# Optimization experiments

Measured on AMD Instinct MI355X. Metric: run time of the kernel, lower is better.

Reference implementation:

```python
import jax, jax.numpy as jnp
import numpy as np

MAX_LEN, BATCH, EMB = 512, 32, 41
HID, UNITS = 800, 20
BOND_LENS = jnp.array([1.329, 1.459, 1.525], jnp.float32)
BOND_ANGLES = jnp.array([2.034, 2.119, 1.937], jnp.float32)
INIT_ABC = jnp.array([[0.0, 0.0, 1.0], [0.0, 1.0, 0.0], [1.0, 0.0, 0.0]], jnp.float32)


def _lstm_dir(x, w_ih, w_hh, b, reverse):
    # x: [T, B, in]; returns hidden states [T, B, H]
    T, B, _ = x.shape
    H = w_hh.shape[1]
    xs = jnp.flip(x, 0) if reverse else x
    xw = jnp.einsum('tbi,gi->tbg', xs, w_ih) + b  # precompute input projection

    def step(carry, xt):
        h, c = carry
        gates = xt + h @ w_hh.T
        i, f, g, o = jnp.split(gates, 4, axis=-1)
        c = jax.nn.sigmoid(f) * c + jax.nn.sigmoid(i) * jnp.tanh(g)
        h = jax.nn.sigmoid(o) * jnp.tanh(c)
        return (h, c), h

    init = (jnp.zeros((B, H), x.dtype), jnp.zeros((B, H), x.dtype))
    _, hs = jax.lax.scan(step, init, xw)
    return jnp.flip(hs, 0) if reverse else hs


def _bilstm_layer(x, w_ih, w_hh, b):
    # w_ih: [2, 4H, in]; w_hh: [2, 4H, H]; b: [2, 4H]
    fwd = _lstm_dir(x, w_ih[0], w_hh[0], b[0], False)
    bwd = _lstm_dir(x, w_ih[1], w_hh[1], b[1], True)
    return jnp.concatenate([fwd, bwd], axis=-1)


def _geometric_unit(coords3, triplet):
    # coords3: [3, B, 3] last three atoms; triplet: [B, 3] torsion angles
    A, Bc, C = coords3[0], coords3[1], coords3[2]
    new = []
    for i in range(3):
        Tang, R, P = BOND_ANGLES[i], BOND_LENS[i], triplet[:, i]
        D2 = jnp.stack([-R * jnp.cos(Tang) * jnp.ones_like(P),
                        R * jnp.cos(P) * jnp.sin(Tang),
                        R * jnp.sin(P) * jnp.sin(Tang)], axis=1)  # [B,3]
        BC = C - Bc
        bc = BC / jnp.linalg.norm(BC, axis=1, keepdims=True)
        AB = Bc - A
        N = jnp.cross(AB, bc)
        n = N / jnp.linalg.norm(N, axis=1, keepdims=True)
        M = jnp.stack([bc, jnp.cross(n, bc), n], axis=2)  # [B,3,3]
        D = jnp.einsum('bij,bj->bi', M, D2) + C
        A, Bc, C = Bc, C, D
        new.append(D)
    return jnp.stack([A, Bc, C]), jnp.stack(new)  # carry, [3,B,3]


def setup_inputs() -> dict:
    key = jax.random.key(0)
    ks = jax.random.split(key, 10)
    k = 1.0 / np.sqrt(HID)
    u = lambda kk, shp, lim: jax.random.uniform(kk, shp, jnp.float32, -lim, lim)
    in0, in1 = EMB + 1, 2 * HID
    return {
        'sequences': jax.random.normal(ks[0], (MAX_LEN, BATCH, EMB), jnp.float32),
        'lengths': jnp.full((BATCH,), MAX_LEN, jnp.int64 if jax.config.jax_enable_x64 else jnp.int32),
        'w_ih0': u(ks[1], (2, 4 * HID, in0), k),
        'w_hh0': u(ks[2], (2, 4 * HID, HID), k),
        'b0': u(ks[3], (2, 4 * HID), k),
        'w_ih1': u(ks[4], (2, 4 * HID, in1), k),
        'w_hh1': u(ks[5], (2, 4 * HID, HID), k),
        'b1': u(ks[6], (2, 4 * HID), k),
        'lin_w': u(ks[7], (UNITS, 2 * HID), 1.0 / np.sqrt(2 * HID)),
        'lin_b': u(ks[8], (UNITS,), 1.0 / np.sqrt(2 * HID)),
        'alphabet': jax.random.uniform(ks[9], (UNITS, 3), jnp.float32, -3.14, 3.14),
    }


def reference(sequences, lengths, w_ih0, w_hh0, b0, w_ih1, w_hh1, b1, lin_w, lin_b, alphabet):
    T, B, _ = sequences.shape
    abs_pos = jnp.broadcast_to(jnp.arange(T, dtype=sequences.dtype)[:, None, None], (T, B, 1))
    x = jnp.concatenate([sequences, abs_pos], axis=2)  # [T, B, EMB+1]
    # 2-layer bidirectional LSTM (all lengths == max_len -> packing is identity)
    h = _bilstm_layer(x, w_ih0, w_hh0, b0)
    h = _bilstm_layer(h, w_ih1, w_hh1, b1)  # [T, B, 2H]
    # linear -> softmax over alphabet, trig angle decode
    soft = jax.nn.softmax(h @ lin_w.T + lin_b, axis=2)  # [T, B, UNITS]
    sine = soft @ jnp.sin(alphabet)   # [T, B, 3]
    cosine = soft @ jnp.cos(alphabet)
    out = jnp.arctan2(sine, cosine)   # torsion angle triplets
    # sequential geometric coordinate recurrence over timesteps 1..T-1
    init = jnp.broadcast_to(INIT_ABC[:, None, :], (3, B, 3))
    _, new_coords = jax.lax.scan(_geometric_unit, init, out[1:])  # [T-1, 3, B, 3]
    pred_coords = jnp.concatenate([init, new_coords.reshape(-1, B, 3)], axis=0)
    return pred_coords  # [3 + 3*(T-1), B, 3]
```

## Files before the change

kernel.cpp:

```cpp
#include <hip/hip_runtime.h>
#include <math.h>

#define T_LEN 512
#define NB    32
#define EMB_  41
#define IN0_  42
#define HID_  800
#define G4_   3200
#define IN1_  1600
#define NU    20
#define NCH0  50
#define NCH   100

typedef unsigned short u16;
typedef unsigned int   u32;
typedef unsigned long long u64;
typedef __attribute__((ext_vector_type(8))) short short8;
typedef __attribute__((ext_vector_type(4))) float f32x4;

__device__ __forceinline__ float bf2f(u16 v) {
    union { u32 u; float f; } c; c.u = ((u32)v) << 16; return c.f;
}
__device__ __forceinline__ u16 f2bf(float f) {
    union { float f; u32 u; } c; c.f = f;
    u32 r = (c.u + 0x7fffu + ((c.u >> 16) & 1u)) >> 16;
    return (u16)r;
}
__device__ __forceinline__ short cvt_hl(float v, int hl) {
    u16 hi = f2bf(v);
    return hl ? (short)f2bf(v - bf2f(hi)) : (short)hi;
}
__device__ __forceinline__ f32x4 mfma16(short8 a, short8 b, f32x4 c) {
    return __builtin_amdgcn_mfma_f32_16x16x32_bf16(a, b, c, 0, 0, 0);
}
__device__ __forceinline__ void astore(u64* p, u64 v) {
    __hip_atomic_store(p, v, __ATOMIC_RELAXED, __HIP_MEMORY_SCOPE_AGENT);
}
__device__ __forceinline__ int afload(const int* p) {
    return __hip_atomic_load(p, __ATOMIC_RELAXED, __HIP_MEMORY_SCOPE_AGENT);
}
__device__ __forceinline__ void afstore(int* p, int v) {
    __hip_atomic_store(p, v, __ATOMIC_RELAXED, __HIP_MEMORY_SCOPE_AGENT);
}


__global__ __launch_bounds__(256, 1)
void lstm0_persist(const float* __restrict__ seq, const float* __restrict__ wih0,
                   const float* __restrict__ whh0, const float* __restrict__ bias,
                   u16* __restrict__ h0f, int* __restrict__ flags)
{
    __shared__ __align__(16) float part[4096];
    __shared__ __align__(16) u16 stageB[25600];
    __shared__ __align__(16) float w0l[64*48];
    __shared__ __align__(16) float xsl[2][32*48];
    __shared__ u16 hpk[2][NB*8];
    const int tid = threadIdx.x;
    const int d = blockIdx.x / NCH0, ch = blockIdx.x % NCH0;
    const int w = tid >> 6, l = tid & 63;
    const int p = w & 1, hl = w >> 1;
    int* myflags = flags + d*128;

    short8 wreg[2][25];
    {
        const int m = l & 15, g = p*2 + (m>>3);
#pragma unroll
        for (int T = 0; T < 2; ++T) {
            const int j = (ch*2 + T)*8 + (m&7);
            const float* base = whh0 + ((size_t)(d*G4_ + g*HID_ + j))*HID_ + (l>>4)*8;
#pragma unroll
            for (int kc = 0; kc < 25; ++kc) {
                float4 f0 = *(const float4*)(base + kc*32);
                float4 f1 = *(const float4*)(base + kc*32 + 4);
                short8 v;
                v[0]=cvt_hl(f0.x,hl); v[1]=cvt_hl(f0.y,hl); v[2]=cvt_hl(f0.z,hl); v[3]=cvt_hl(f0.w,hl);
                v[4]=cvt_hl(f1.x,hl); v[5]=cvt_hl(f1.y,hl); v[6]=cvt_hl(f1.z,hl); v[7]=cvt_hl(f1.w,hl);
                wreg[T][kc] = v;
            }
        }
    }
    for (int idx = tid; idx < 64*EMB_; idx += 256) {
        int r = idx / EMB_, k = idx % EMB_;
        int ju_ = r >> 2, g = r & 3;
        w0l[r*48 + k] = wih0[((size_t)(d*G4_ + g*HID_ + ch*16 + ju_))*IN0_ + k];
    }
    const int ju = tid >> 5, b = tid & 31;
    const int nt = b >> 4, n = b & 15;
    float biasr[2][4], wpos[2][4];
#pragma unroll
    for (int T = 0; T < 2; ++T) {
        const int j = ch*16 + T*8 + ju;
#pragma unroll
        for (int g = 0; g < 4; ++g) {
            biasr[T][g] = bias[d*G4_ + g*HID_ + j];
            wpos[T][g]  = wih0[((size_t)(d*G4_ + g*HID_ + j))*IN0_ + EMB_];
        }
    }
    float creg[2] = {0.f, 0.f};
    __syncthreads();

    for (int s = 0; s < T_LEN; ++s) {
        const int t = d ? (T_LEN-1-s) : s;

        for (int idx = tid; idx < 32*EMB_; idx += 256)
            xsl[s&1][(idx/EMB_)*48 + idx%EMB_] = seq[(size_t)t*(NB*EMB_) + idx];

        if (s > 0 && tid < NCH0)
            while (afload(myflags + tid) < s) __builtin_amdgcn_s_sleep(1);
        __syncthreads();

        if (s == 0) {
#pragma unroll
            for (int q = 0; q < 25; ++q) ((u64*)stageB)[tid + q*256] = 0ull;
        } else {
            const int tprev = d ? (T_LEN - s) : (s - 1);
            const u64* src = (const u64*)(h0f + (size_t)tprev*51200) + d*6400;
            u64 tmp[25];
#pragma unroll
            for (int q = 0; q < 25; ++q) tmp[q] = src[tid + q*256];
#pragma unroll
            for (int q = 0; q < 25; ++q) ((u64*)stageB)[tid + q*256] = tmp[q];
        }
        __syncthreads();

        f32x4 a00 = {0.f,0.f,0.f,0.f}, a01 = {0.f,0.f,0.f,0.f};
        f32x4 a10 = {0.f,0.f,0.f,0.f}, a11 = {0.f,0.f,0.f,0.f};
#pragma unroll
        for (int kc = 0; kc < 25; ++kc) {
            short8 b0 = *(const short8*)(stageB + kc*1024 + l*8);
            short8 b1 = *(const short8*)(stageB + kc*1024 + 512 + l*8);
            a00 = mfma16(wreg[0][kc], b0, a00);
            a01 = mfma16(wreg[0][kc], b1, a01);
            a10 = mfma16(wreg[1][kc], b0, a10);
            a11 = mfma16(wreg[1][kc], b1, a11);
        }
        {
            const int mrow = (l>>4)*4, nn = l & 15;
#pragma unroll
            for (int r = 0; r < 4; ++r) {
                part[((0*8 + (p*2+hl)*2 + 0)*16 + mrow + r)*16 + nn] = a00[r];
                part[((0*8 + (p*2+hl)*2 + 1)*16 + mrow + r)*16 + nn] = a01[r];
                part[((1*8 + (p*2+hl)*2 + 0)*16 + mrow + r)*16 + nn] = a10[r];
                part[((1*8 + (p*2+hl)*2 + 1)*16 + mrow + r)*16 + nn] = a11[r];
            }
        }
        __syncthreads();

#pragma unroll
        for (int T = 0; T < 2; ++T) {
            float dot0 = 0.f, dot1 = 0.f, dot2 = 0.f, dot3 = 0.f;
            const float* wr = &w0l[(T*8 + ju)*4*48];
            const float* xr = &xsl[s&1][b*48];
#pragma unroll
            for (int k4 = 0; k4 < 40; k4 += 4) {
                float4 xk = *(const float4*)(xr + k4);
                float4 w0 = *(const float4*)(wr + 0*48 + k4);
                float4 w1 = *(const float4*)(wr + 1*48 + k4);
                float4 w2 = *(const float4*)(wr + 2*48 + k4);
                float4 w3 = *(const float4*)(wr + 3*48 + k4);
                dot0 += w0.x*xk.x + w0.y*xk.y + w0.z*xk.z + w0.w*xk.w;
                dot1 += w1.x*xk.x + w1.y*xk.y + w1.z*xk.z + w1.w*xk.w;
                dot2 += w2.x*xk.x + w2.y*xk.y + w2.z*xk.z + w2.w*xk.w;
                dot3 += w3.x*xk.x + w3.y*xk.y + w3.z*xk.z + w3.w*xk.w;
            }
            float xk = xr[40];
            dot0 += wr[0*48+40]*xk; dot1 += wr[1*48+40]*xk;
            dot2 += wr[2*48+40]*xk; dot3 += wr[3*48+40]*xk;
            float v[4] = {dot0, dot1, dot2, dot3};
#pragma unroll
            for (int g = 0; g < 4; ++g) {
                const int pp = g >> 1, m = (g & 1)*8 + ju;
                v[g] += part[((T*8 + (pp*2+0)*2 + nt)*16 + m)*16 + n]
                      + part[((T*8 + (pp*2+1)*2 + nt)*16 + m)*16 + n]
                      + biasr[T][g] + (float)t * wpos[T][g];
            }
            float ig = 1.f/(1.f + expf(-v[0]));
            float fg = 1.f/(1.f + expf(-v[1]));
            float gg = tanhf(v[2]);
            float og = 1.f/(1.f + expf(-v[3]));
            creg[T] = fg * creg[T] + ig * gg;
            hpk[T][b*8 + ju] = f2bf(og * tanhf(creg[T]));
        }
        __syncthreads();

        if (tid < 128) {
            const int T = tid >> 6, tl = tid & 63;
            const int bb = tl >> 1, half = tl & 1;
            const u16* hp = &hpk[T][bb*8 + half*4];
            u64 pk = (u64)hp[0] | ((u64)hp[1]<<16) | ((u64)hp[2]<<32) | ((u64)hp[3]<<48);
            const int ch2 = ch*2 + T;
            const int ntb = bb >> 4, llb = ((ch2&3)<<4) | (bb&15);
            const int xoff = ((d*25 + (ch2>>2))*2 + ntb)*128 + llb*2 + half;
            astore((u64*)(h0f + (size_t)t*51200) + xoff, pk);
        }
        __syncthreads();
        if (tid == 0) afstore(myflags + ch, s+1);
    }
}

__global__ __launch_bounds__(256, 1)
void lstm1_persist(const float* __restrict__ wih1, const float* __restrict__ whh1,
                   const float* __restrict__ bias, const float* __restrict__ lin_w,
                   const u16* __restrict__ h0f, u16* __restrict__ h1f,
                   int* __restrict__ flags, float* __restrict__ logits)
{
    __shared__ __align__(16) u16 wihL[2*50*512];
    __shared__ __align__(16) u16 stageB[25600];
    __shared__ __align__(16) float part[2048];
    __shared__ u16 hpk[NB*8];
    const int tid = threadIdx.x;
    const int d = blockIdx.x / NCH, ch = blockIdx.x % NCH;
    const int w = tid >> 6, l = tid & 63;
    const int p = w & 1, hl = w >> 1;
    int* myflags = flags + d*128;

    short8 wreg[25];
    {
        const int m = l & 15, g = p*2 + (m>>3), j = ch*8 + (m&7);
        const float* base = whh1 + ((size_t)(d*G4_ + g*HID_ + j))*HID_ + (l>>4)*8;
#pragma unroll
        for (int kc = 0; kc < 25; ++kc) {
            float4 f0 = *(const float4*)(base + kc*32);
            float4 f1 = *(const float4*)(base + kc*32 + 4);
            short8 v;
            v[0]=cvt_hl(f0.x,hl); v[1]=cvt_hl(f0.y,hl); v[2]=cvt_hl(f0.z,hl); v[3]=cvt_hl(f0.w,hl);
            v[4]=cvt_hl(f1.x,hl); v[5]=cvt_hl(f1.y,hl); v[6]=cvt_hl(f1.z,hl); v[7]=cvt_hl(f1.w,hl);
            wreg[kc] = v;
        }
    }
    for (int o = tid; o < 6400; o += 256) {
        int pp = o / 3200, r = o % 3200, kc = r >> 6, ll = r & 63;
        int m = ll & 15, g = pp*2 + (m>>3), jj = ch*8 + (m&7);
        const float* base = wih1 + ((size_t)(d*G4_ + g*HID_ + jj))*IN1_ + kc*32 + (ll>>4)*8;
        float4 f0 = *(const float4*)base;
        float4 f1 = *(const float4*)(base + 4);
        short8 v;
        v[0]=(short)f2bf(f0.x); v[1]=(short)f2bf(f0.y); v[2]=(short)f2bf(f0.z); v[3]=(short)f2bf(f0.w);
        v[4]=(short)f2bf(f1.x); v[5]=(short)f2bf(f1.y); v[6]=(short)f2bf(f1.z); v[7]=(short)f2bf(f1.w);
        *(short8*)&wihL[o*8] = v;
    }
    const int ol = tid >> 5, ln = tid & 31;
    const int lo = ch*7 + ol;
    const bool lown = (ol < 7) && (lo < NB*NU);
    int lofs = 0;
    float wlin[25];
    if (lown) {
        const int bb = lo / NU, uu = lo % NU;
        lofs = (bb >> 4)*512 + ((((ln >> 3) << 4) | (bb & 15)))*8 + (ln & 7);
        const float* wrow = lin_w + (size_t)uu*IN1_ + d*HID_ + ln;
#pragma unroll
        for (int i = 0; i < 25; ++i) wlin[i] = wrow[i*32];
    }
    const int ju = tid >> 5, b = tid & 31;
    const int j = ch*8 + ju;
    const int nt = b >> 4, n = b & 15;
    float biasr[4];
#pragma unroll
    for (int g = 0; g < 4; ++g) biasr[g] = bias[d*G4_ + g*HID_ + j];
    float creg = 0.f;
    __syncthreads();

    for (int s = 0; s < T_LEN; ++s) {
        const int t = d ? (T_LEN-1-s) : s;

        f32x4 acc0 = {0.f,0.f,0.f,0.f}, acc1 = {0.f,0.f,0.f,0.f};
        {
            const u16* xb = h0f + (size_t)t*51200;
#pragma unroll 5
            for (int kc = 0; kc < 25; ++kc) {
                const int idx = hl*25 + kc;
                short8 a  = *(const short8*)&wihL[(p*50 + idx)*512 + l*8];
                short8 b0 = *(const short8*)(xb + idx*1024 + l*8);
                short8 b1 = *(const short8*)(xb + idx*1024 + 512 + l*8);
                acc0 = mfma16(a, b0, acc0);
                acc1 = mfma16(a, b1, acc1);
            }
        }

        if (s > 0 && tid < NCH)
            while (afload(myflags + tid) < s) __builtin_amdgcn_s_sleep(1);
        __syncthreads();

        if (s == 0) {
#pragma unroll
            for (int q = 0; q < 25; ++q) ((u64*)stageB)[tid + q*256] = 0ull;
        } else {
            const int tprev = d ? (T_LEN - s) : (s - 1);
            const u64* src = (const u64*)(h1f + (size_t)tprev*51200) + d*6400;
            u64 tmp[25];
#pragma unroll
            for (int q = 0; q < 25; ++q) tmp[q] = src[tid + q*256];
#pragma unroll
            for (int q = 0; q < 25; ++q) ((u64*)stageB)[tid + q*256] = tmp[q];
        }
        __syncthreads();

#pragma unroll 5
        for (int kc = 0; kc < 25; ++kc) {
            short8 b0 = *(const short8*)(stageB + kc*1024 + l*8);
            short8 b1 = *(const short8*)(stageB + kc*1024 + 512 + l*8);
            acc0 = mfma16(wreg[kc], b0, acc0);
            acc1 = mfma16(wreg[kc], b1, acc1);
        }
        {
            const int mrow = (l>>4)*4, nn = l & 15;
#pragma unroll
            for (int r = 0; r < 4; ++r) {
                part[(((p*2+hl)*2 + 0)*16 + mrow + r)*16 + nn] = acc0[r];
                part[(((p*2+hl)*2 + 1)*16 + mrow + r)*16 + nn] = acc1[r];
            }
        }
        __syncthreads();

        float v[4];
#pragma unroll
        for (int g = 0; g < 4; ++g) {
            const int pp = g >> 1, m = (g & 1)*8 + ju;
            v[g] = part[(((pp*2+0)*2 + nt)*16 + m)*16 + n]
                 + part[(((pp*2+1)*2 + nt)*16 + m)*16 + n] + biasr[g];
        }
        float ig = 1.f/(1.f + expf(-v[0]));
        float fg = 1.f/(1.f + expf(-v[1]));
        float gg = tanhf(v[2]);
        float og = 1.f/(1.f + expf(-v[3]));
        creg = fg * creg + ig * gg;
        float hn = og * tanhf(creg);
        hpk[b*8 + ju] = f2bf(hn);
        __syncthreads();

        if (tid < 64) {
            const int bb = tid >> 1, half = tid & 1;
            const u16* hp = &hpk[bb*8 + half*4];
            u64 pk = (u64)hp[0] | ((u64)hp[1]<<16) | ((u64)hp[2]<<32) | ((u64)hp[3]<<48);
            const int ntb = bb >> 4, llb = ((ch&3)<<4) | (bb&15);
            const int xoff = ((d*25 + (ch>>2))*2 + ntb)*128 + llb*2 + half;
            astore((u64*)(h1f + (size_t)t*51200) + xoff, pk);
        }
        __syncthreads();
        if (tid == 0) afstore(myflags + ch, s+1);

        if (s > 0 && lown) {
            float sum = 0.f;
#pragma unroll
            for (int i = 0; i < 25; ++i)
                sum += bf2f(stageB[i*1024 + lofs]) * wlin[i];
#pragma unroll
            for (int off2 = 16; off2; off2 >>= 1) sum += __shfl_down(sum, off2, 32);
            if (ln == 0) {
                const int tprev = d ? (T_LEN - s) : (s - 1);
                logits[((size_t)d*T_LEN + tprev)*640 + lo] = sum;
            }
        }
    }
    if (tid < NCH)
        while (afload(myflags + tid) < T_LEN) __builtin_amdgcn_s_sleep(1);
    __syncthreads();
    {
        const int tlast = d ? 0 : (T_LEN - 1);
        const u64* src = (const u64*)(h1f + (size_t)tlast*51200) + d*6400;
        u64 tmp[25];
#pragma unroll
        for (int q = 0; q < 25; ++q) tmp[q] = src[tid + q*256];
#pragma unroll
        for (int q = 0; q < 25; ++q) ((u64*)stageB)[tid + q*256] = tmp[q];
    }
    __syncthreads();
    if (lown) {
        float sum = 0.f;
#pragma unroll
        for (int i = 0; i < 25; ++i)
            sum += bf2f(stageB[i*1024 + lofs]) * wlin[i];
#pragma unroll
        for (int off2 = 16; off2; off2 >>= 1) sum += __shfl_down(sum, off2, 32);
        if (ln == 0) {
            const int tprev = d ? 0 : (T_LEN - 1);
            logits[((size_t)d*T_LEN + tprev)*640 + lo] = sum;
        }
    }
}

__global__ __launch_bounds__(256)
void epilogue(const float* __restrict__ logits, const float* __restrict__ lin_b,
              const float* __restrict__ alphabet, float* __restrict__ cs)
{
    __shared__ float sa[NU*3], ca[NU*3], lb[NU];
    const int tid = threadIdx.x;
    if (tid < NU*3) { float al = alphabet[tid]; sa[tid] = sinf(al); ca[tid] = cosf(al); }
    if (tid < NU) lb[tid] = lin_b[tid];
    __syncthreads();
    const int row = blockIdx.x*256 + tid;
    if (row >= T_LEN*NB) return;
    const int t = row >> 5, b = row & 31;
    float lg[NU];
    float m = -1e30f;
#pragma unroll 4
    for (int u = 0; u < NU; ++u) {
        lg[u] = lb[u] + logits[(size_t)t*640 + b*NU + u]
                      + logits[((size_t)T_LEN + t)*640 + b*NU + u];
        m = fmaxf(m, lg[u]);
    }
    float ssum = 0.f;
#pragma unroll 4
    for (int u = 0; u < NU; ++u) { lg[u] = expf(lg[u] - m); ssum += lg[u]; }
    float inv = 1.f / ssum;
#pragma unroll
    for (int i = 0; i < 3; ++i) {
        float sv = 0.f, cv = 0.f;
#pragma unroll 4
        for (int u = 0; u < NU; ++u) {
            float sw = lg[u] * inv;
            sv += sw * sa[u*3 + i];
            cv += sw * ca[u*3 + i];
        }
        float rinv = rsqrtf(fmaxf(sv*sv + cv*cv, 1e-30f));
        *(float2*)(cs + ((size_t)row*3 + i)*2) = make_float2(cv*rinv, sv*rinv);
    }
}

__global__ __launch_bounds__(64)
void geometry(const float* __restrict__ cs, float* __restrict__ out)
{
    const int b = threadIdx.x;
    if (b >= NB) return;
    const float blen[3] = {1.329f, 1.459f, 1.525f};
    const float bang[3] = {2.034f, 2.119f, 1.937f};
    float sT[3], cT[3];
#pragma unroll
    for (int i = 0; i < 3; ++i) { sT[i] = sinf(bang[i]); cT[i] = cosf(bang[i]); }

    float Ax=0.f,Ay=0.f,Az=1.f, Bx=0.f,By=1.f,Bz=0.f, Cx=1.f,Cy=0.f,Cz=0.f;
    out[(0*NB + b)*3 + 0] = 0.f; out[(0*NB + b)*3 + 1] = 0.f; out[(0*NB + b)*3 + 2] = 1.f;
    out[(1*NB + b)*3 + 0] = 0.f; out[(1*NB + b)*3 + 1] = 1.f; out[(1*NB + b)*3 + 2] = 0.f;
    out[(2*NB + b)*3 + 0] = 1.f; out[(2*NB + b)*3 + 1] = 0.f; out[(2*NB + b)*3 + 2] = 0.f;

    for (int t = 1; t < T_LEN; ++t) {
        float2 pc[3];
#pragma unroll
        for (int i = 0; i < 3; ++i)
            pc[i] = *(const float2*)(cs + (((size_t)t*NB + b)*3 + i)*2);
#pragma unroll
        for (int i = 0; i < 3; ++i) {
            float R = blen[i];
            float d2x = -R*cT[i], d2y = R*pc[i].x*sT[i], d2z = R*pc[i].y*sT[i];
            float bcx = Cx-Bx, bcy = Cy-By, bcz = Cz-Bz;
            float inv = rsqrtf(bcx*bcx + bcy*bcy + bcz*bcz);
            bcx *= inv; bcy *= inv; bcz *= inv;
            float abx = Bx-Ax, aby = By-Ay, abz = Bz-Az;
            float nx = aby*bcz - abz*bcy;
            float ny = abz*bcx - abx*bcz;
            float nz = abx*bcy - aby*bcx;
            inv = rsqrtf(fmaxf(nx*nx + ny*ny + nz*nz, 1e-30f));
            nx *= inv; ny *= inv; nz *= inv;
            float mx = ny*bcz - nz*bcy;
            float my = nz*bcx - nx*bcz;
            float mz = nx*bcy - ny*bcx;
            float Dx = bcx*d2x + mx*d2y + nx*d2z + Cx;
            float Dy = bcy*d2x + my*d2y + ny*d2z + Cy;
            float Dz = bcz*d2x + mz*d2y + nz*d2z + Cz;
            Ax=Bx; Ay=By; Az=Bz; Bx=Cx; By=Cy; Bz=Cz; Cx=Dx; Cy=Dy; Cz=Dz;
            const int r = 3 + (t-1)*3 + i;
            out[((size_t)r*NB + b)*3 + 0] = Dx;
            out[((size_t)r*NB + b)*3 + 1] = Dy;
            out[((size_t)r*NB + b)*3 + 2] = Dz;
        }
    }
}

extern "C" void kernel_launch(void* const* d_in, const int* in_sizes, int n_in,
                              void* d_out, int out_size, void* d_ws, size_t ws_size,
                              hipStream_t stream)
{
    (void)in_sizes; (void)n_in; (void)out_size; (void)ws_size;
    const float* seq   = (const float*)d_in[0];
    const float* w_ih0 = (const float*)d_in[2];
    const float* w_hh0 = (const float*)d_in[3];
    const float* b0    = (const float*)d_in[4];
    const float* w_ih1 = (const float*)d_in[5];
    const float* w_hh1 = (const float*)d_in[6];
    const float* b1    = (const float*)d_in[7];
    const float* lin_w = (const float*)d_in[8];
    const float* lin_b = (const float*)d_in[9];
    const float* alpha = (const float*)d_in[10];

    char* ws = (char*)d_ws;
    size_t off = 0;
    u16* h0f   = (u16*)(ws + off); off += 52428800ull;
    u16* h1f   = (u16*)(ws + off); off += 52428800ull;
    int* flagsL0 = (int*)(ws + off); off += 1024ull;
    int* flagsL1 = (int*)(ws + off); off += 1024ull;
    float* logits = (float*)(ws + off); off += 2621440ull;
    float* cs = (float*)(ws + off); off += 393216ull;

    hipMemsetAsync(flagsL0, 0, 2048, stream);

    lstm0_persist<<<dim3(2*NCH0), dim3(256), 0, stream>>>(seq, w_ih0, w_hh0, b0, h0f, flagsL0);

    lstm1_persist<<<dim3(2*NCH), dim3(256), 0, stream>>>(w_ih1, w_hh1, b1, lin_w, h0f, h1f,
                                                         flagsL1, logits);

    epilogue<<<dim3(64), dim3(256), 0, stream>>>(logits, lin_b, alpha, cs);
    geometry<<<dim3(1), dim3(64), 0, stream>>>(cs, (float*)d_out);
}
```

Measured before the change: 9.321 ms.

## Split layer-1 LSTM into producer blocks computing input projection ahead of recurrence

Adds lstm1_fast, which launches 400 blocks. 200 producer blocks hold W_ih1 in registers, compute the layer-1 input projection per timestep, and write it to a large fp32 workspace buffer behind per-block progress flags. The other 200 recurrent blocks keep only W_hh1 in registers and read the precomputed projection, so the serial per-step critical path no longer includes the input GEMM. The fast path needs about 530MB of workspace and falls back to the old kernel otherwise. It relies on all 400 blocks being co-resident for the spin-waits to make progress, and it adds substantial global memory traffic.

```diff
diff --git a/kernel.cpp b/kernel.cpp
--- a/kernel.cpp
+++ b/kernel.cpp
@@ -194,6 +194,224 @@
         }
         __syncthreads();
         if (tid == 0) afstore(myflags + ch, s+1);
+    }
+}
+
+__global__ __launch_bounds__(256, 1)
+void lstm1_fast(const float* __restrict__ whh1, const float* __restrict__ wih1,
+                const float* __restrict__ bias, const float* __restrict__ lin_w,
+                const u16* __restrict__ h0f, u16* __restrict__ h1f,
+                float* __restrict__ xwv, int* __restrict__ flags,
+                int* __restrict__ prodflag, float* __restrict__ logits)
+{
+    __shared__ __align__(16) u16 stageB[25600];
+    __shared__ __align__(16) float part[2048];
+    __shared__ u16 hpk[NB*8];
+    const int tid = threadIdx.x;
+    const int w = tid >> 6, l = tid & 63;
+    const int p = w & 1, hl = w >> 1;
+    const int ju = tid >> 5, b = tid & 31;
+    const int nt = b >> 4, n = b & 15;
+
+    if (blockIdx.x < 200) {
+        const int dq = blockIdx.x / 100, ch = blockIdx.x % 100;
+        short8 wregx[25];
+        {
+            const int m = l & 15, g = p*2 + (m>>3), jj = ch*8 + (m&7);
+            const float* basew = wih1 + ((size_t)(dq*G4_ + g*HID_ + jj))*IN1_ + (l>>4)*8;
+#pragma unroll
+            for (int kc = 0; kc < 25; ++kc) {
+                const int idx = hl*25 + kc;
+                float4 f0 = *(const float4*)(basew + idx*32);
+                float4 f1 = *(const float4*)(basew + idx*32 + 4);
+                short8 v;
+                v[0]=(short)f2bf(f0.x); v[1]=(short)f2bf(f0.y); v[2]=(short)f2bf(f0.z); v[3]=(short)f2bf(f0.w);
+                v[4]=(short)f2bf(f1.x); v[5]=(short)f2bf(f1.y); v[6]=(short)f2bf(f1.z); v[7]=(short)f2bf(f1.w);
+                wregx[kc] = v;
+            }
+        }
+        int* pf = prodflag + blockIdx.x;
+        for (int k = 0; k < T_LEN; ++k) {
+            const int t = dq ? (T_LEN-1-k) : k;
+            const u16* xb = h0f + (size_t)t*51200;
+            f32x4 a0 = {0.f,0.f,0.f,0.f}, a1 = {0.f,0.f,0.f,0.f};
+#pragma unroll 5
+            for (int kc = 0; kc < 25; ++kc) {
+                const int idx = hl*25 + kc;
+                short8 b0 = *(const short8*)(xb + idx*1024 + l*8);
+                short8 b1 = *(const short8*)(xb + idx*1024 + 512 + l*8);
+                a0 = mfma16(wregx[kc], b0, a0);
+                a1 = mfma16(wregx[kc], b1, a1);
+            }
+            {
+                const int mrow = (l>>4)*4, nn = l & 15;
+#pragma unroll
+                for (int r = 0; r < 4; ++r) {
+                    part[(((p*2+hl)*2 + 0)*16 + mrow + r)*16 + nn] = a0[r];
+                    part[(((p*2+hl)*2 + 1)*16 + mrow + r)*16 + nn] = a1[r];
+                }
+            }
+            __syncthreads();
+            union { float f[4]; u64 q[2]; } uo;
+#pragma unroll
+            for (int g = 0; g < 4; ++g) {
+                const int pp = g >> 1, m = (g & 1)*8 + ju;
+                uo.f[g] = part[(((pp*2+0)*2 + nt)*16 + m)*16 + n]
+                        + part[(((pp*2+1)*2 + nt)*16 + m)*16 + n];
+            }
+            u64* dst = (u64*)xwv + ((((size_t)dq*100 + ch)*T_LEN + t)*256 + tid)*2;
+            astore(dst, uo.q[0]);
+            astore(dst + 1, uo.q[1]);
+            __syncthreads();
+            if (tid == 0) afstore(pf, k+1);
+        }
+        return;
+    }
+
+    const int d = (blockIdx.x - 200) / 100, ch = (blockIdx.x - 200) % 100;
+    int* myflags = flags + d*128;
+    const int* pf = prodflag + d*100 + ch;
+
+    short8 wreg[25];
+    {
+        const int m = l & 15, g = p*2 + (m>>3), j = ch*8 + (m&7);
+        const float* base = whh1 + ((size_t)(d*G4_ + g*HID_ + j))*HID_ + (l>>4)*8;
+#pragma unroll
+        for (int kc = 0; kc < 25; ++kc) {
+            float4 f0 = *(const float4*)(base + kc*32);
+            float4 f1 = *(const float4*)(base + kc*32 + 4);
+            short8 v;
+            v[0]=cvt_hl(f0.x,hl); v[1]=cvt_hl(f0.y,hl); v[2]=cvt_hl(f0.z,hl); v[3]=cvt_hl(f0.w,hl);
+            v[4]=cvt_hl(f1.x,hl); v[5]=cvt_hl(f1.y,hl); v[6]=cvt_hl(f1.z,hl); v[7]=cvt_hl(f1.w,hl);
+            wreg[kc] = v;
+        }
+    }
+    const int ol = tid >> 5, ln = tid & 31;
+    const int lo = ch*7 + ol;
+    const bool lown = (ol < 7) && (lo < NB*NU);
+    int lofs = 0;
+    float wlin[25];
+    if (lown) {
+        const int bb = lo / NU, uu = lo % NU;
+        lofs = (bb >> 4)*512 + ((((ln >> 3) << 4) | (bb & 15)))*8 + (ln & 7);
+        const float* wrow = lin_w + (size_t)uu*IN1_ + d*HID_ + ln;
+#pragma unroll
+        for (int i = 0; i < 25; ++i) wlin[i] = wrow[i*32];
+    }
+    const int j = ch*8 + ju;
+    float biasr[4];
+#pragma unroll
+    for (int g = 0; g < 4; ++g) biasr[g] = bias[d*G4_ + g*HID_ + j];
+    float creg = 0.f;
+    __syncthreads();
+
+    for (int s = 0; s < T_LEN; ++s) {
+        const int t = d ? (T_LEN-1-s) : s;
+
+        if (s > 0 && tid < NCH)
+            while (afload(myflags + tid) < s) __builtin_amdgcn_s_sleep(1);
+        if (tid == 128)
+            while (afload(pf) < s+1) __builtin_amdgcn_s_sleep(1);
+        __syncthreads();
+
+        float4 xq = *(const float4*)(xwv + ((((size_t)d*100 + ch)*T_LEN + t)*256 + tid)*4);
+        if (s == 0) {
+#pragma unroll
+            for (int q = 0; q < 25; ++q) ((u64*)stageB)[tid + q*256] = 0ull;
+        } else {
+            const int tprev = d ? (T_LEN - s) : (s - 1);
+            const u64* src = (const u64*)(h1f + (size_t)tprev*51200) + d*6400;
+            u64 tmp[25];
+#pragma unroll
+            for (int q = 0; q < 25; ++q) tmp[q] = src[tid + q*256];
+#pragma unroll
+            for (int q = 0; q < 25; ++q) ((u64*)stageB)[tid + q*256] = tmp[q];
+        }
+        __syncthreads();
+
+        f32x4 acc0 = {0.f,0.f,0.f,0.f}, acc1 = {0.f,0.f,0.f,0.f};
+#pragma unroll 5
+        for (int kc = 0; kc < 25; ++kc) {
+            short8 b0 = *(const short8*)(stageB + kc*1024 + l*8);
+            short8 b1 = *(const short8*)(stageB + kc*1024 + 512 + l*8);
+            acc0 = mfma16(wreg[kc], b0, acc0);
+            acc1 = mfma16(wreg[kc], b1, acc1);
+        }
+        {
+            const int mrow = (l>>4)*4, nn = l & 15;
+#pragma unroll
+            for (int r = 0; r < 4; ++r) {
+                part[(((p*2+hl)*2 + 0)*16 + mrow + r)*16 + nn] = acc0[r];
+                part[(((p*2+hl)*2 + 1)*16 + mrow + r)*16 + nn] = acc1[r];
+            }
+        }
+        __syncthreads();
+
+        float xqa[4] = {xq.x, xq.y, xq.z, xq.w};
+        float v[4];
+#pragma unroll
+        for (int g = 0; g < 4; ++g) {
+            const int pp = g >> 1, m = (g & 1)*8 + ju;
+            v[g] = part[(((pp*2+0)*2 + nt)*16 + m)*16 + n]
+                 + part[(((pp*2+1)*2 + nt)*16 + m)*16 + n] + xqa[g] + biasr[g];
+        }
+        float ig = 1.f/(1.f + expf(-v[0]));
+        float fg = 1.f/(1.f + expf(-v[1]));
+        float gg = tanhf(v[2]);
+        float og = 1.f/(1.f + expf(-v[3]));
+        creg = fg * creg + ig * gg;
+        float hn = og * tanhf(creg);
+        hpk[b*8 + ju] = f2bf(hn);
+        __syncthreads();
+
+        if (tid < 64) {
+            const int bb = tid >> 1, half = tid & 1;
+            const u16* hp = &hpk[bb*8 + half*4];
+            u64 pk = (u64)hp[0] | ((u64)hp[1]<<16) | ((u64)hp[2]<<32) | ((u64)hp[3]<<48);
+            const int ntb = bb >> 4, llb = ((ch&3)<<4) | (bb&15);
+            const int xoff = ((d*25 + (ch>>2))*2 + ntb)*128 + llb*2 + half;
+            astore((u64*)(h1f + (size_t)t*51200) + xoff, pk);
+        }
+        __syncthreads();
+        if (tid == 0) afstore(myflags + ch, s+1);
+
+        if (s > 0 && lown) {
+            float sum = 0.f;
+#pragma unroll
+            for (int i = 0; i < 25; ++i)
+                sum += bf2f(stageB[i*1024 + lofs]) * wlin[i];
+#pragma unroll
+            for (int off2 = 16; off2; off2 >>= 1) sum += __shfl_down(sum, off2, 32);
+            if (ln == 0) {
+                const int tprev = d ? (T_LEN - s) : (s - 1);
+                logits[((size_t)d*T_LEN + tprev)*640 + lo] = sum;
+            }
+        }
+    }
+    if (tid < NCH)
+        while (afload(myflags + tid) < T_LEN) __builtin_amdgcn_s_sleep(1);
+    __syncthreads();
+    {
+        const int tlast = d ? 0 : (T_LEN - 1);
+        const u64* src = (const u64*)(h1f + (size_t)tlast*51200) + d*6400;
+        u64 tmp[25];
+#pragma unroll
+        for (int q = 0; q < 25; ++q) tmp[q] = src[tid + q*256];
+#pragma unroll
+        for (int q = 0; q < 25; ++q) ((u64*)stageB)[tid + q*256] = tmp[q];
+    }
+    __syncthreads();
+    if (lown) {
+        float sum = 0.f;
+#pragma unroll
+        for (int i = 0; i < 25; ++i)
+            sum += bf2f(stageB[i*1024 + lofs]) * wlin[i];
+#pragma unroll
+        for (int off2 = 16; off2; off2 >>= 1) sum += __shfl_down(sum, off2, 32);
+        if (ln == 0) {
+            const int tprev = d ? 0 : (T_LEN - 1);
+            logits[((size_t)d*T_LEN + tprev)*640 + lo] = sum;
+        }
     }
 }
 
@@ -469,7 +687,7 @@
                               void* d_out, int out_size, void* d_ws, size_t ws_size,
                               hipStream_t stream)
 {
-    (void)in_sizes; (void)n_in; (void)out_size; (void)ws_size;
+    (void)in_sizes; (void)n_in; (void)out_size;
     const float* seq   = (const float*)d_in[0];
     const float* w_ih0 = (const float*)d_in[2];
     const float* w_hh0 = (const float*)d_in[3];
@@ -482,21 +700,43 @@
     const float* alpha = (const float*)d_in[10];
 
     char* ws = (char*)d_ws;
-    size_t off = 0;
-    u16* h0f   = (u16*)(ws + off); off += 52428800ull;
-    u16* h1f   = (u16*)(ws + off); off += 52428800ull;
-    int* flagsL0 = (int*)(ws + off); off += 1024ull;
-    int* flagsL1 = (int*)(ws + off); off += 1024ull;
-    float* logits = (float*)(ws + off); off += 2621440ull;
-    float* cs = (float*)(ws + off); off += 393216ull;
-
-    hipMemsetAsync(flagsL0, 0, 2048, stream);
-
-    lstm0_persist<<<dim3(2*NCH0), dim3(256), 0, stream>>>(seq, w_ih0, w_hh0, b0, h0f, flagsL0);
-
-    lstm1_persist<<<dim3(2*NCH), dim3(256), 0, stream>>>(w_ih1, w_hh1, b1, lin_w, h0f, h1f,
-                                                         flagsL1, logits);
-
-    epilogue<<<dim3(64), dim3(256), 0, stream>>>(logits, lin_b, alpha, cs);
-    geometry<<<dim3(1), dim3(64), 0, stream>>>(cs, (float*)d_out);
-}
+    const bool fastp = (ws_size >= 530000000ull);
+
+    if (fastp) {
+        size_t off = 0;
+        u16* h0f      = (u16*)(ws + off); off += 52428800ull;
+        u16* h1f      = (u16*)(ws + off); off += 52428800ull;
+        float* xwv    = (float*)(ws + off); off += 419430400ull;
+        int* flagsL0  = (int*)(ws + off); off += 1024ull;
+        int* flagsL1  = (int*)(ws + off); off += 1024ull;
+        int* prodflag = (int*)(ws + off); off += 1024ull;
+        float* logits = (float*)(ws + off); off += 2621440ull;
+        float* cs     = (float*)(ws + off); off += 393216ull;
+
+        hipMemsetAsync(flagsL0, 0, 3072, stream);
+
+        lstm0_persist<<<dim3(2*NCH0), dim3(256), 0, stream>>>(seq, w_ih0, w_hh0, b0,
+                                                              h0f, flagsL0);
+        lstm1_fast<<<dim3(400), dim3(256), 0, stream>>>(w_hh1, w_ih1, b1, lin_w, h0f, h1f,
+                                                        xwv, flagsL1, prodflag, logits);
+        epilogue<<<dim3(64), dim3(256), 0, stream>>>(logits, lin_b, alpha, cs);
+        geometry<<<dim3(1), dim3(64), 0, stream>>>(cs, (float*)d_out);
+    } else {
+        size_t off = 0;
+        u16* h0f      = (u16*)(ws + off); off += 52428800ull;
+        u16* h1f      = (u16*)(ws + off); off += 52428800ull;
+        int* flagsL0  = (int*)(ws + off); off += 1024ull;
+        int* flagsL1  = (int*)(ws + off); off += 1024ull;
+        float* logits = (float*)(ws + off); off += 2621440ull;
+        float* cs     = (float*)(ws + off); off += 393216ull;
+
+        hipMemsetAsync(flagsL0, 0, 2048, stream);
+
+        lstm0_persist<<<dim3(2*NCH0), dim3(256), 0, stream>>>(seq, w_ih0, w_hh0, b0,
+                                                              h0f, flagsL0);
+        lstm1_persist<<<dim3(2*NCH), dim3(256), 0, stream>>>(w_ih1, w_hh1, b1, lin_w,
+                                                             h0f, h1f, flagsL1, logits);
+        epilogue<<<dim3(64), dim3(256), 0, stream>>>(logits, lin_b, alpha, cs);
+        geometry<<<dim3(1), dim3(64), 0, stream>>>(cs, (float*)d_out);
+    }
+}
```

New measurement: 9.326 ms. About the same (+0.1%).

## Offload layer-1 input projection to producer blocks via ring buffer

Applied to the files above, without the earlier changes.

Splits the layer-1 LSTM kernel into 200 producer blocks that compute the input projection W_ih·h0 per timestep and 200 consumer blocks that run the recurrence. Data passes through a 16-slot global ring buffer guarded by produce and acknowledge flags. This takes the input-projection MFMAs and the large W_ih LDS tile off the serial recurrence path, so each recurrent step only does the W_hh product plus a small load. The cost is 400 co-resident persistent blocks, which could deadlock if not all are resident at once, plus extra flag polling and global traffic.

```diff
diff --git a/kernel.cpp b/kernel.cpp
--- a/kernel.cpp
+++ b/kernel.cpp
@@ -11,6 +11,7 @@
 #define NU    20
 #define NCH0  50
 #define NCH   100
+#define RING  16
 
 typedef unsigned short u16;
 typedef unsigned int   u32;
@@ -35,6 +36,9 @@
 }
 __device__ __forceinline__ void astore(u64* p, u64 v) {
     __hip_atomic_store(p, v, __ATOMIC_RELAXED, __HIP_MEMORY_SCOPE_AGENT);
+}
+__device__ __forceinline__ u64 aload(const u64* p) {
+    return __hip_atomic_load(p, __ATOMIC_RELAXED, __HIP_MEMORY_SCOPE_AGENT);
 }
 __device__ __forceinline__ int afload(const int* p) {
     return __hip_atomic_load(p, __ATOMIC_RELAXED, __HIP_MEMORY_SCOPE_AGENT);
@@ -198,20 +202,87 @@
 }
 
 __global__ __launch_bounds__(256, 1)
-void lstm1_persist(const float* __restrict__ wih1, const float* __restrict__ whh1,
-                   const float* __restrict__ bias, const float* __restrict__ lin_w,
-                   const u16* __restrict__ h0f, u16* __restrict__ h1f,
-                   int* __restrict__ flags, float* __restrict__ logits)
+void lstm1_fast(const float* __restrict__ whh1, const float* __restrict__ wih1,
+                const float* __restrict__ bias, const float* __restrict__ lin_w,
+                const u16* __restrict__ h0f, u16* __restrict__ h1f,
+                float* __restrict__ xwv, int* __restrict__ flags,
+                int* __restrict__ prodflag, int* __restrict__ ackf,
+                float* __restrict__ logits)
 {
-    __shared__ __align__(16) u16 wihL[2*50*512];
     __shared__ __align__(16) u16 stageB[25600];
     __shared__ __align__(16) float part[2048];
     __shared__ u16 hpk[NB*8];
     const int tid = threadIdx.x;
-    const int d = blockIdx.x / NCH, ch = blockIdx.x % NCH;
     const int w = tid >> 6, l = tid & 63;
     const int p = w & 1, hl = w >> 1;
+    const int ju = tid >> 5, b = tid & 31;
+    const int nt = b >> 4, n = b & 15;
+
+    if (blockIdx.x < 200) {
+        const int dq = blockIdx.x / 100, chq = blockIdx.x % 100;
+        short8 wregx[25];
+        {
+            const int m = l & 15, g = p*2 + (m>>3), jj = chq*8 + (m&7);
+            const float* basew = wih1 + ((size_t)(dq*G4_ + g*HID_ + jj))*IN1_ + (l>>4)*8;
+#pragma unroll
+            for (int kc = 0; kc < 25; ++kc) {
+                const int idx = hl*25 + kc;
+                float4 f0 = *(const float4*)(basew + idx*32);
+                float4 f1 = *(const float4*)(basew + idx*32 + 4);
+                short8 v;
+                v[0]=(short)f2bf(f0.x); v[1]=(short)f2bf(f0.y); v[2]=(short)f2bf(f0.z); v[3]=(short)f2bf(f0.w);
+                v[4]=(short)f2bf(f1.x); v[5]=(short)f2bf(f1.y); v[6]=(short)f2bf(f1.z); v[7]=(short)f2bf(f1.w);
+                wregx[kc] = v;
+            }
+        }
+        int* pf = prodflag + blockIdx.x;
+        const int* ackp = ackf + blockIdx.x;
+        for (int k = 0; k < T_LEN; ++k) {
+            const int t = dq ? (T_LEN-1-k) : k;
+            if (k >= RING) {
+                if (tid == 0)
+                    while (afload(ackp) < k - RING + 1) __builtin_amdgcn_s_sleep(1);
+                __syncthreads();
+            }
+            const u16* xb = h0f + (size_t)t*51200;
+            f32x4 a0 = {0.f,0.f,0.f,0.f}, a1 = {0.f,0.f,0.f,0.f};
+#pragma unroll 5
+            for (int kc = 0; kc < 25; ++kc) {
+                const int idx = hl*25 + kc;
+                short8 b0 = *(const short8*)(xb + idx*1024 + l*8);
+                short8 b1 = *(const short8*)(xb + idx*1024 + 512 + l*8);
+                a0 = mfma16(wregx[kc], b0, a0);
+                a1 = mfma16(wregx[kc], b1, a1);
+            }
+            {
+                const int mrow = (l>>4)*4, nn = l & 15;
+#pragma unroll
+                for (int r = 0; r < 4; ++r) {
+                    part[(((p*2+hl)*2 + 0)*16 + mrow + r)*16 + nn] = a0[r];
+                    part[(((p*2+hl)*2 + 1)*16 + mrow + r)*16 + nn] = a1[r];
+                }
+            }
+            __syncthreads();
+            union { float f[4]; u64 q[2]; } uo;
+#pragma unroll
+            for (int g = 0; g < 4; ++g) {
+                const int pp = g >> 1, m = (g & 1)*8 + ju;
+                uo.f[g] = part[(((pp*2+0)*2 + nt)*16 + m)*16 + n]
+                        + part[(((pp*2+1)*2 + nt)*16 + m)*16 + n];
+            }
+            u64* dst = (u64*)xwv + (((size_t)(dq*100 + chq)*RING + (k & (RING-1)))*256 + tid)*2;
+            astore(dst, uo.q[0]);
+            astore(dst + 1, uo.q[1]);
+            __syncthreads();
+            if (tid == 0) afstore(pf, k+1);
+        }
+        return;
+    }
+
+    const int d = (blockIdx.x - 200) / 100, ch = (blockIdx.x - 200) % 100;
     int* myflags = flags + d*128;
+    const int* pf = prodflag + d*100 + ch;
+    int* myack = ackf + d*100 + ch;
 
     short8 wreg[25];
     {
@@ -226,17 +297,6 @@
             v[4]=cvt_hl(f1.x,hl); v[5]=cvt_hl(f1.y,hl); v[6]=cvt_hl(f1.z,hl); v[7]=cvt_hl(f1.w,hl);
             wreg[kc] = v;
         }
-    }
-    for (int o = tid; o < 6400; o += 256) {
-        int pp = o / 3200, r = o % 3200, kc = r >> 6, ll = r & 63;
-        int m = ll & 15, g = pp*2 + (m>>3), jj = ch*8 + (m&7);
-        const float* base = wih1 + ((size_t)(d*G4_ + g*HID_ + jj))*IN1_ + kc*32 + (ll>>4)*8;
-        float4 f0 = *(const float4*)base;
-        float4 f1 = *(const float4*)(base + 4);
-        short8 v;
-        v[0]=(short)f2bf(f0.x); v[1]=(short)f2bf(f0.y); v[2]=(short)f2bf(f0.z); v[3]=(short)f2bf(f0.w);
-        v[4]=(short)f2bf(f1.x); v[5]=(short)f2bf(f1.y); v[6]=(short)f2bf(f1.z); v[7]=(short)f2bf(f1.w);
-        *(short8*)&wihL[o*8] = v;
     }
     const int ol = tid >> 5, ln = tid & 31;
     const int lo = ch*7 + ol;
@@ -250,9 +310,7 @@
 #pragma unroll
         for (int i = 0; i < 25; ++i) wlin[i] = wrow[i*32];
     }
-    const int ju = tid >> 5, b = tid & 31;
     const int j = ch*8 + ju;
-    const int nt = b >> 4, n = b & 15;
     float biasr[4];
 #pragma unroll
     for (int g = 0; g < 4; ++g) biasr[g] = bias[d*G4_ + g*HID_ + j];
@@ -262,24 +320,19 @@
     for (int s = 0; s < T_LEN; ++s) {
         const int t = d ? (T_LEN-1-s) : s;
 
-        f32x4 acc0 = {0.f,0.f,0.f,0.f}, acc1 = {0.f,0.f,0.f,0.f};
-        {
-            const u16* xb = h0f + (size_t)t*51200;
-#pragma unroll 5
-            for (int kc = 0; kc < 25; ++kc) {
-                const int idx = hl*25 + kc;
-                short8 a  = *(const short8*)&wihL[(p*50 + idx)*512 + l*8];
-                short8 b0 = *(const short8*)(xb + idx*1024 + l*8);
-                short8 b1 = *(const short8*)(xb + idx*1024 + 512 + l*8);
-                acc0 = mfma16(a, b0, acc0);
-                acc1 = mfma16(a, b1, acc1);
-            }
-        }
-
         if (s > 0 && tid < NCH)
             while (afload(myflags + tid) < s) __builtin_amdgcn_s_sleep(1);
-        __syncthreads();
-
+        if (tid == 128)
+            while (afload(pf) < s+1) __builtin_amdgcn_s_sleep(1);
+        __syncthreads();
+
+        u64 xq0, xq1;
+        {
+            const u64* src = (const u64*)xwv +
+                (((size_t)(d*100 + ch)*RING + (s & (RING-1)))*256 + tid)*2;
+            xq0 = aload(src);
+            xq1 = aload(src + 1);
+        }
         if (s == 0) {
 #pragma unroll
             for (int q = 0; q < 25; ++q) ((u64*)stageB)[tid + q*256] = 0ull;
@@ -294,6 +347,7 @@
         }
         __syncthreads();
 
+        f32x4 acc0 = {0.f,0.f,0.f,0.f}, acc1 = {0.f,0.f,0.f,0.f};
 #pragma unroll 5
         for (int kc = 0; kc < 25; ++kc) {
             short8 b0 = *(const short8*)(stageB + kc*1024 + l*8);
@@ -311,12 +365,14 @@
         }
         __syncthreads();
 
+        union { u64 q[2]; float f[4]; } xu;
+        xu.q[0] = xq0; xu.q[1] = xq1;
         float v[4];
 #pragma unroll
         for (int g = 0; g < 4; ++g) {
             const int pp = g >> 1, m = (g & 1)*8 + ju;
             v[g] = part[(((pp*2+0)*2 + nt)*16 + m)*16 + n]
-                 + part[(((pp*2+1)*2 + nt)*16 + m)*16 + n] + biasr[g];
+                 + part[(((pp*2+1)*2 + nt)*16 + m)*16 + n] + xu.f[g] + biasr[g];
         }
         float ig = 1.f/(1.f + expf(-v[0]));
         float fg = 1.f/(1.f + expf(-v[1]));
@@ -336,7 +392,10 @@
             astore((u64*)(h1f + (size_t)t*51200) + xoff, pk);
         }
         __syncthreads();
-        if (tid == 0) afstore(myflags + ch, s+1);
+        if (tid == 0) {
+            afstore(myflags + ch, s+1);
+            afstore(myack, s+1);
+        }
 
         if (s > 0 && lown) {
             float sum = 0.f;
@@ -483,19 +542,23 @@
 
     char* ws = (char*)d_ws;
     size_t off = 0;
-    u16* h0f   = (u16*)(ws + off); off += 52428800ull;
-    u16* h1f   = (u16*)(ws + off); off += 52428800ull;
-    int* flagsL0 = (int*)(ws + off); off += 1024ull;
-    int* flagsL1 = (int*)(ws + off); off += 1024ull;
+    u16* h0f      = (u16*)(ws + off); off += 52428800ull;
+    u16* h1f      = (u16*)(ws + off); off += 52428800ull;
+    float* xwv    = (float*)(ws + off); off += 13107200ull;
+    int* flagsL0  = (int*)(ws + off); off += 1024ull;
+    int* flagsL1  = (int*)(ws + off); off += 1024ull;
+    int* prodflag = (int*)(ws + off); off += 1024ull;
+    int* ackf     = (int*)(ws + off); off += 1024ull;
     float* logits = (float*)(ws + off); off += 2621440ull;
-    float* cs = (float*)(ws + off); off += 393216ull;
-
-    hipMemsetAsync(flagsL0, 0, 2048, stream);
-
-    lstm0_persist<<<dim3(2*NCH0), dim3(256), 0, stream>>>(seq, w_ih0, w_hh0, b0, h0f, flagsL0);
-
-    lstm1_persist<<<dim3(2*NCH), dim3(256), 0, stream>>>(w_ih1, w_hh1, b1, lin_w, h0f, h1f,
-                                                         flagsL1, logits);
+    float* cs     = (float*)(ws + off); off += 393216ull;
+
+    hipMemsetAsync(flagsL0, 0, 4096, stream);
+
+    lstm0_persist<<<dim3(2*NCH0), dim3(256), 0, stream>>>(seq, w_ih0, w_hh0, b0,
+                                                          h0f, flagsL0);
+
+    lstm1_fast<<<dim3(400), dim3(256), 0, stream>>>(w_hh1, w_ih1, b1, lin_w, h0f, h1f,
+                                                    xwv, flagsL1, prodflag, ackf, logits);
 
     epilogue<<<dim3(64), dim3(256), 0, stream>>>(logits, lin_b, alpha, cs);
     geometry<<<dim3(1), dim3(64), 0, stream>>>(cs, (float*)d_out);
```

Result: slower. 11.61 ms (+24.5%).
